# Performance work log

Hardware: AMD Instinct MI355X
Metric: run time of the kernel (lower is better)

Reference implementation:

```python
import jax, jax.numpy as jnp
import numpy as np

Nx, Nu, Ny, Np, H = 2, 1, 2, 8, 32
Nz = Np * (Nx + Nu)  # 24
B, T = 4096, 256
F, V, Delta = 0.1, 1.0, 1.0  # ps.squeeze(), volume, sample time
ymean = jnp.array([0.5, 0.5], jnp.float32)
ystd = jnp.array([0.3, 0.2], jnp.float32)
umean = jnp.array([1.0], jnp.float32)
ustd = jnp.array([0.5], jnp.float32)


def fnn(x, params):
    # dense layers: tanh hidden, linear output
    for W, b in params[:-1]:
        x = jnp.tanh(x @ W + b)
    W, b = params[-1]
    return x @ W + b


def fxzu(x, z, u, p1, p2, p3):
    # dCa/dt = F*(Caf-Ca)/V - r1 ; dCb/dt = -F*Cb/V + r1 - 3*r2 + r3
    Castd, Cbstd = ystd[0:1], ystd[1:2]
    r1 = fnn(x[:, 0:1], p1) * Castd
    r2 = fnn(x[:, 1:2], p2) * Cbstd
    r3 = fnn(z, p3) * Cbstd
    xs = x * ystd + ymean
    us = u * ustd + umean
    Ca, Cb, Caf = xs[:, 0:1], xs[:, 1:2], us[:, 0:1]
    dCa = F * (Caf - Ca) / V - r1
    dCb = -F * Cb / V + r1 - 3.0 * r2 + r3
    return jnp.concatenate([dCa, dCb], axis=-1) / ystd


def interp(yseq):
    # (B,(Np+1)*Nx) -> (B, Np*Nx): midpoints of consecutive Nx-blocks
    b = yseq.shape[0]
    y = yseq.reshape(b, Np + 1, Nx)
    return (0.5 * (y[:, :-1] + y[:, 1:])).reshape(b, Np * Nx)


def run(useq, xz0, p1, p2, p3):
    def step(xz, u):
        x, z = xz[:, :Nx], xz[:, Nx:]
        xpseq, upseq = z[:, :Np * Nx], z[:, Np * Nx:]
        k1 = fxzu(x, z, u, p1, p2, p3)
        z23 = jnp.concatenate([interp(jnp.concatenate([xpseq, x], -1)), upseq], -1)
        k2 = fxzu(x + Delta * k1 / 2, z23, u, p1, p2, p3)
        k3 = fxzu(x + Delta * k2 / 2, z23, u, p1, p2, p3)
        z4 = jnp.concatenate([xpseq[:, Nx:], x, upseq], -1)
        k4 = fxzu(x + Delta * k3, z4, u, p1, p2, p3)
        xplus = x + (Delta / 6.0) * (k1 + 2 * k2 + 2 * k3 + k4)
        zplus = jnp.concatenate([xpseq[:, Nx:], x, upseq[:, Nu:], u], -1)
        return jnp.concatenate([xplus, zplus], -1), x  # output is pre-update x
    _, ys = jax.lax.scan(step, xz0, jnp.swapaxes(useq, 0, 1))
    return jnp.swapaxes(ys, 0, 1)  # (B, T, Ny)


def setup_inputs() -> dict:
    key = jax.random.key(0)
    ks = jax.random.split(key, 12)
    inp = {
        'useq': jax.random.normal(ks[0], (B, T, Nu), jnp.float32),
        'xz0': jax.random.normal(ks[1], (B, Nx + Nz), jnp.float32),
    }
    dims = {'r1': [1, H, H, 1], 'r2': [1, H, H, 1], 'r3': [Nz, H, H, 1]}
    i = 2
    for name, ds in dims.items():
        for l, (din, dout) in enumerate(zip(ds[:-1], ds[1:])):
            inp[f'{name}W{l}'] = jax.random.normal(ks[i], (din, dout), jnp.float32) / np.sqrt(din).astype(np.float32)
            inp[f'{name}b{l}'] = jnp.zeros((dout,), jnp.float32)
            i += 1
    return inp


def reference(useq, xz0, r1W0, r1b0, r1W1, r1b1, r1W2, r1b2,
              r2W0, r2b0, r2W1, r2b1, r2W2, r2b2,
              r3W0, r3b0, r3W1, r3b1, r3W2, r3b2):
    p1 = [(r1W0, r1b0), (r1W1, r1b1), (r1W2, r1b2)]
    p2 = [(r2W0, r2b0), (r2W1, r2b1), (r2W2, r2b2)]
    p3 = [(r3W0, r3b0), (r3W1, r3b1), (r3W2, r3b2)]
    return run(useq, xz0, p1, p2, p3)
```

## Files before the change

### kernel.cpp

```cpp
#include <hip/hip_runtime.h>

#define DEVINL static __device__ __forceinline__
#define LDSBAR() asm volatile("s_waitcnt lgkmcnt(0)" ::: "memory")

typedef float v2f __attribute__((ext_vector_type(2)));

DEVINL v2f mk2(float a, float b) { v2f r; r.x = a; r.y = b; return r; }
DEVINL v2f pkfma(v2f a, v2f b, v2f c) { return __builtin_elementwise_fma(a, b, c); }

DEVINL float tanh_fast(float x) {
  float e = __expf(2.0f * x);
  return 1.0f - 2.0f * __builtin_amdgcn_rcpf(e + 1.0f);
}

template <int CTRL>
DEVINL float dpp_add(float v) {
  int t = __builtin_amdgcn_update_dpp(0, __float_as_int(v), CTRL, 0xF, 0xF, true);
  return v + __int_as_float(t);
}
DEVINL float rsum32(float v) {
  v = dpp_add<0xB1>(v);
  v = dpp_add<0x4E>(v);
  v = dpp_add<0x141>(v);
  v = dpp_add<0x140>(v);
  v += __int_as_float(__builtin_amdgcn_ds_swizzle(__float_as_int(v), 0x401F));
  return v;
}

DEVINL float dot32(const float* hrow, const v2f* W, float bias) {
  const float4* hp = (const float4*)hrow;
  v2f a0 = mk2(bias, 0.f), a1 = mk2(0.f, 0.f);
  v2f a2 = mk2(0.f, 0.f), a3 = mk2(0.f, 0.f);
#pragma unroll
  for (int q = 0; q < 8; q += 2) {
    float4 x = hp[q], y = hp[q + 1];
    a0 = pkfma(mk2(x.x, x.y), W[2 * q + 0], a0);
    a1 = pkfma(mk2(x.z, x.w), W[2 * q + 1], a1);
    a2 = pkfma(mk2(y.x, y.y), W[2 * q + 2], a2);
    a3 = pkfma(mk2(y.z, y.w), W[2 * q + 3], a3);
  }
  v2f s = (a0 + a1) + (a2 + a3);
  return s.x + s.y;
}
DEVINL float pdot16(const float* hrow, const v2f* W) {
  const float4* hp = (const float4*)hrow;
  v2f a0 = mk2(0.f, 0.f), a1 = mk2(0.f, 0.f);
  float4 x = hp[0], y = hp[1];
  a0 = pkfma(mk2(x.x, x.y), W[0], a0);
  a1 = pkfma(mk2(x.z, x.w), W[1], a1);
  a0 = pkfma(mk2(y.x, y.y), W[2], a0);
  a1 = pkfma(mk2(y.z, y.w), W[3], a1);
  x = hp[2]; y = hp[3];
  a0 = pkfma(mk2(x.x, x.y), W[4], a0);
  a1 = pkfma(mk2(x.z, x.w), W[5], a1);
  a0 = pkfma(mk2(y.x, y.y), W[6], a0);
  a1 = pkfma(mk2(y.z, y.w), W[7], a1);
  v2f s = a0 + a1;
  return s.x + s.y;
}

constexpr int TSTEPS = 256;

__global__ __launch_bounds__(64, 4) void reac_kernel(
    const float* __restrict__ useq,
    const float* __restrict__ xz0,
    const float* __restrict__ r1W0, const float* __restrict__ r1b0,
    const float* __restrict__ r1W1, const float* __restrict__ r1b1,
    const float* __restrict__ r1W2, const float* __restrict__ r1b2,
    const float* __restrict__ r2W0, const float* __restrict__ r2b0,
    const float* __restrict__ r2W1, const float* __restrict__ r2b1,
    const float* __restrict__ r2W2, const float* __restrict__ r2b2,
    const float* __restrict__ r3W0, const float* __restrict__ r3b0,
    const float* __restrict__ r3W1, const float* __restrict__ r3b1,
    const float* __restrict__ r3W2, const float* __restrict__ r3b2,
    float2* __restrict__ out)
{
  const int lane = threadIdx.x;
  const int j = lane & 31;
  const bool hi = lane >= 32;
  const int b = blockIdx.x;

  const float* W0p = hi ? r2W0 : r1W0;
  const float* B0p = hi ? r2b0 : r1b0;
  const float* W1p = hi ? r2W1 : r1W1;
  const float* B1p = hi ? r2b1 : r1b1;
  const float* W2p = hi ? r2W2 : r1W2;
  const float* B2p = hi ? r2b2 : r1b2;
  float w0 = W0p[j], b0 = B0p[j], b1 = B1p[j], w2 = W2p[j], b2 = B2p[0];
  float sc = hi ? 0.2f : 0.3f;

  v2f W1v[16];
#pragma unroll
  for (int k = 0; k < 16; ++k)
    W1v[k] = mk2(W1p[(2 * k) * 32 + j], W1p[(2 * k + 1) * 32 + j]);

  v2f W0Cv[12];
#pragma unroll
  for (int m = 0; m < 12; ++m)
    W0Cv[m] = mk2(r3W0[(2 * m) * 32 + j], r3W0[(2 * m + 1) * 32 + j]);
  const int kbase = hi ? 16 : 0;
  v2f W1Cv[8];
#pragma unroll
  for (int k = 0; k < 8; ++k)
    W1Cv[k] = mk2(r3W1[(kbase + 2 * k) * 32 + j],
                  r3W1[(kbase + 2 * k + 1) * 32 + j]);
  float b0C = r3b0[j], b1C = r3b1[j], w2C = r3W2[j], b2C = r3b2[0];

  __shared__ __align__(16) float zs[24];
  __shared__ __align__(16) float zb[16];
  __shared__ __align__(16) float h12[2][32];
  __shared__ __align__(16) float hR3[3][32];

  float x0 = xz0[b * 26 + 0];
  float x1 = xz0[b * 26 + 1];
  if (!hi && j < 24) zs[j] = xz0[b * 26 + 2 + j];
  LDSBAR();

  auto stage = [&](float sxv, float syv, float rc, float Caf,
                   float& kx, float& ky) {
    float s = hi ? syv : sxv;
    float h = tanh_fast(fmaf(s, w0, b0));
    LDSBAR();
    h12[hi][j] = h;
    LDSBAR();
    float a = dot32(&h12[hi][0], W1v, b1);
    float r = (rsum32(tanh_fast(a) * w2) + b2) * sc;
    float rp = __shfl_xor(r, 32);
    float ra = hi ? rp : r;
    float rb = hi ? r : rp;
    float Ca = fmaf(sxv, 0.3f, 0.5f);
    float Cb = fmaf(syv, 0.2f, 0.5f);
    float dCa = 0.1f * (Caf - Ca) - ra;
    float dCb = fmaf(-0.1f, Cb, ra - 3.0f * rb + rc);
    kx = dCa * (1.0f / 0.3f);
    ky = dCb * (1.0f / 0.2f);
  };

  float u = useq[b * TSTEPS];

  for (int t = 0; t < TSTEPS; ++t) {
    int tn = (t < TSTEPS - 1) ? (t + 1) : t;
    float u_nxt = useq[b * TSTEPS + tn];
    float Caf = fmaf(u, 0.5f, 1.0f);

    if (lane == 0) out[b * TSTEPS + t] = make_float2(x0, x1);

    if (!hi && j < 16) {
      zb[j] = (j < 14) ? zs[j + 2] : ((j == 14) ? x0 : x1);
    }
    LDSBAR();

    const float4* zp = (const float4*)(hi ? &zb[0] : &zs[0]);
    float4 z0 = zp[0], z1 = zp[1], z2 = zp[2], z3 = zp[3];
    const float4* up = (const float4*)&zs[16];
    float4 u0 = up[0], u1 = up[1];
    v2f aa = mk2(b0C, 0.f), ab = mk2(0.f, 0.f);
    aa = pkfma(mk2(z0.x, z0.y), W0Cv[0], aa);
    ab = pkfma(mk2(z0.z, z0.w), W0Cv[1], ab);
    aa = pkfma(mk2(z1.x, z1.y), W0Cv[2], aa);
    ab = pkfma(mk2(z1.z, z1.w), W0Cv[3], ab);
    aa = pkfma(mk2(z2.x, z2.y), W0Cv[4], aa);
    ab = pkfma(mk2(z2.z, z2.w), W0Cv[5], ab);
    aa = pkfma(mk2(z3.x, z3.y), W0Cv[6], aa);
    ab = pkfma(mk2(z3.z, z3.w), W0Cv[7], ab);
    aa = pkfma(mk2(u0.x, u0.y), W0Cv[8], aa);
    ab = pkfma(mk2(u0.z, u0.w), W0Cv[9], ab);
    aa = pkfma(mk2(u1.x, u1.y), W0Cv[10], aa);
    ab = pkfma(mk2(u1.z, u1.w), W0Cv[11], ab);
    v2f as = aa + ab;
    float A = as.x + as.y;
    float Ap = __shfl_xor(A, 32);
    float tA = tanh_fast(A);
    if (!hi) {
      hR3[0][j] = tA;
      hR3[1][j] = tanh_fast(0.5f * (A + Ap));
    } else {
      hR3[2][j] = tA;
    }
    LDSBAR();
    float p0 = pdot16(&hR3[0][kbase], W1Cv);
    float p1 = pdot16(&hR3[1][kbase], W1Cv);
    float p2 = pdot16(&hR3[2][kbase], W1Cv);
    float o0 = p0 + __shfl_xor(p0, 32) + b1C;
    float o1 = p1 + __shfl_xor(p1, 32) + b1C;
    float o2 = p2 + __shfl_xor(p2, 32) + b1C;
    float rc1  = (rsum32(tanh_fast(o0) * w2C) + b2C) * 0.2f;
    float rc23 = (rsum32(tanh_fast(o1) * w2C) + b2C) * 0.2f;
    float rc4  = (rsum32(tanh_fast(o2) * w2C) + b2C) * 0.2f;

    float kx1, ky1, kx2, ky2, kx3, ky3, kx4, ky4;
    stage(x0, x1, rc1, Caf, kx1, ky1);
    stage(fmaf(kx1, 0.5f, x0), fmaf(ky1, 0.5f, x1), rc23, Caf, kx2, ky2);
    stage(fmaf(kx2, 0.5f, x0), fmaf(ky2, 0.5f, x1), rc23, Caf, kx3, ky3);
    stage(x0 + kx3, x1 + ky3, rc4, Caf, kx4, ky4);

    float znew = 0.0f;
    bool updz = (!hi) && (j < 24);
    if (updz) znew = (j < 16) ? zb[j] : ((j < 23) ? zs[j + 1] : u);
    LDSBAR();
    if (updz) zs[j] = znew;
    x0 += (kx1 + 2.0f * (kx2 + kx3) + kx4) * (1.0f / 6.0f);
    x1 += (ky1 + 2.0f * (ky2 + ky3) + ky4) * (1.0f / 6.0f);
    u = u_nxt;
    LDSBAR();
  }
}

extern "C" void kernel_launch(void* const* d_in, const int* in_sizes, int n_in,
                              void* d_out, int out_size, void* d_ws, size_t ws_size,
                              hipStream_t stream) {
  const float* p[20];
  for (int i = 0; i < 20; ++i) p[i] = (const float*)d_in[i];
  reac_kernel<<<dim3(4096), dim3(64), 0, stream>>>(
      p[0], p[1], p[2], p[3], p[4], p[5], p[6], p[7], p[8], p[9], p[10],
      p[11], p[12], p[13], p[14], p[15], p[16], p[17], p[18], p[19],
      (float2*)d_out);
}
```

Measured before the change: 946.6 us.

## Fold tanh exp scaling into weights and drop explicit LDS waitcnt barriers

Pre-multiplies the layer weights and biases by 2*log2(e) so each tanh can call a raw exp2 builtin with no extra multiply. The output scales and affine constants are folded into w2/b2 and the Caf/Ca/Cb terms. The explicit s_waitcnt lgkmcnt(0) fences become compiler-only memory fences, so the compiler places its own waits, and shfl_xor is replaced by a direct ds_bpermute. It also switches to explicit waves_per_eu attributes; the risks are correctness of the intra-wave LDS ordering without explicit waits and small floating-point differences from the refactored arithmetic.

Result: faster. 871.6 us (-7.9%).

```diff
diff --git a/kernel.cpp b/kernel.cpp
--- a/kernel.cpp
+++ b/kernel.cpp
@@ -1,15 +1,23 @@
 #include <hip/hip_runtime.h>
 
 #define DEVINL static __device__ __forceinline__
-#define LDSBAR() asm volatile("s_waitcnt lgkmcnt(0)" ::: "memory")
+#define CFENCE() asm volatile("" ::: "memory")
 
 typedef float v2f __attribute__((ext_vector_type(2)));
 
 DEVINL v2f mk2(float a, float b) { v2f r; r.x = a; r.y = b; return r; }
 DEVINL v2f pkfma(v2f a, v2f b, v2f c) { return __builtin_elementwise_fma(a, b, c); }
 
-DEVINL float tanh_fast(float x) {
-  float e = __expf(2.0f * x);
+constexpr float KE = 2.885390081777927f;
+
+#if __has_builtin(__builtin_amdgcn_exp2f)
+DEVINL float exp2_fast(float x) { return __builtin_amdgcn_exp2f(x); }
+#else
+DEVINL float exp2_fast(float x) { return __expf(x * 0.6931471805599453f); }
+#endif
+
+DEVINL float tanh_pre(float t) {
+  float e = exp2_fast(t);
   return 1.0f - 2.0f * __builtin_amdgcn_rcpf(e + 1.0f);
 }
 
@@ -61,7 +69,8 @@
 
 constexpr int TSTEPS = 256;
 
-__global__ __launch_bounds__(64, 4) void reac_kernel(
+__global__ __attribute__((amdgpu_flat_work_group_size(64, 64)))
+__attribute__((amdgpu_waves_per_eu(4, 4))) void reac_kernel(
     const float* __restrict__ useq,
     const float* __restrict__ xz0,
     const float* __restrict__ r1W0, const float* __restrict__ r1b0,
@@ -79,6 +88,11 @@
   const int j = lane & 31;
   const bool hi = lane >= 32;
   const int b = blockIdx.x;
+  const int xaddr = ((lane ^ 32) << 2);
+
+  auto xchg = [&](float v) -> float {
+    return __int_as_float(__builtin_amdgcn_ds_bpermute(xaddr, __float_as_int(v)));
+  };
 
   const float* W0p = hi ? r2W0 : r1W0;
   const float* B0p = hi ? r2b0 : r1b0;
@@ -86,25 +100,29 @@
   const float* B1p = hi ? r2b1 : r1b1;
   const float* W2p = hi ? r2W2 : r1W2;
   const float* B2p = hi ? r2b2 : r1b2;
-  float w0 = W0p[j], b0 = B0p[j], b1 = B1p[j], w2 = W2p[j], b2 = B2p[0];
-  float sc = hi ? 0.2f : 0.3f;
+  const float sc = hi ? 0.2f : 0.3f;
+  float w0K = W0p[j] * KE, b0K = B0p[j] * KE;
+  float b1K = B1p[j] * KE;
+  float w2sc = W2p[j] * sc, b2sc = B2p[0] * sc;
 
   v2f W1v[16];
 #pragma unroll
   for (int k = 0; k < 16; ++k)
-    W1v[k] = mk2(W1p[(2 * k) * 32 + j], W1p[(2 * k + 1) * 32 + j]);
+    W1v[k] = mk2(W1p[(2 * k) * 32 + j] * KE, W1p[(2 * k + 1) * 32 + j] * KE);
 
   v2f W0Cv[12];
 #pragma unroll
   for (int m = 0; m < 12; ++m)
-    W0Cv[m] = mk2(r3W0[(2 * m) * 32 + j], r3W0[(2 * m + 1) * 32 + j]);
+    W0Cv[m] = mk2(r3W0[(2 * m) * 32 + j] * KE, r3W0[(2 * m + 1) * 32 + j] * KE);
   const int kbase = hi ? 16 : 0;
   v2f W1Cv[8];
 #pragma unroll
   for (int k = 0; k < 8; ++k)
-    W1Cv[k] = mk2(r3W1[(kbase + 2 * k) * 32 + j],
-                  r3W1[(kbase + 2 * k + 1) * 32 + j]);
-  float b0C = r3b0[j], b1C = r3b1[j], w2C = r3W2[j], b2C = r3b2[0];
+    W1Cv[k] = mk2(r3W1[(kbase + 2 * k) * 32 + j] * KE,
+                  r3W1[(kbase + 2 * k + 1) * 32 + j] * KE);
+  float b0CK = r3b0[j] * KE, b1CK = r3b1[j] * KE;
+  float w2C02 = r3W2[j] * 0.2f;
+  float b2Cs = r3b2[0] * 0.2f - 0.05f;
 
   __shared__ __align__(16) float zs[24];
   __shared__ __align__(16) float zb[16];
@@ -114,24 +132,22 @@
   float x0 = xz0[b * 26 + 0];
   float x1 = xz0[b * 26 + 1];
   if (!hi && j < 24) zs[j] = xz0[b * 26 + 2 + j];
-  LDSBAR();
-
-  auto stage = [&](float sxv, float syv, float rc, float Caf,
+  CFENCE();
+
+  auto stage = [&](float sxv, float syv, float rcp_, float CafF,
                    float& kx, float& ky) {
     float s = hi ? syv : sxv;
-    float h = tanh_fast(fmaf(s, w0, b0));
-    LDSBAR();
+    float h = tanh_pre(fmaf(s, w0K, b0K));
+    CFENCE();
     h12[hi][j] = h;
-    LDSBAR();
-    float a = dot32(&h12[hi][0], W1v, b1);
-    float r = (rsum32(tanh_fast(a) * w2) + b2) * sc;
-    float rp = __shfl_xor(r, 32);
+    CFENCE();
+    float a = dot32(&h12[hi][0], W1v, b1K);
+    float r = rsum32(tanh_pre(a) * w2sc) + b2sc;
+    float rp = xchg(r);
     float ra = hi ? rp : r;
     float rb = hi ? r : rp;
-    float Ca = fmaf(sxv, 0.3f, 0.5f);
-    float Cb = fmaf(syv, 0.2f, 0.5f);
-    float dCa = 0.1f * (Caf - Ca) - ra;
-    float dCb = fmaf(-0.1f, Cb, ra - 3.0f * rb + rc);
+    float dCa = fmaf(-0.03f, sxv, CafF) - ra;
+    float dCb = fmaf(-0.02f, syv, fmaf(-3.0f, rb, ra) + rcp_);
     kx = dCa * (1.0f / 0.3f);
     ky = dCb * (1.0f / 0.2f);
   };
@@ -141,20 +157,21 @@
   for (int t = 0; t < TSTEPS; ++t) {
     int tn = (t < TSTEPS - 1) ? (t + 1) : t;
     float u_nxt = useq[b * TSTEPS + tn];
-    float Caf = fmaf(u, 0.5f, 1.0f);
+    float CafF = fmaf(u, 0.05f, 0.05f);
 
     if (lane == 0) out[b * TSTEPS + t] = make_float2(x0, x1);
 
+    CFENCE();
     if (!hi && j < 16) {
       zb[j] = (j < 14) ? zs[j + 2] : ((j == 14) ? x0 : x1);
     }
-    LDSBAR();
+    CFENCE();
 
     const float4* zp = (const float4*)(hi ? &zb[0] : &zs[0]);
     float4 z0 = zp[0], z1 = zp[1], z2 = zp[2], z3 = zp[3];
     const float4* up = (const float4*)&zs[16];
     float4 u0 = up[0], u1 = up[1];
-    v2f aa = mk2(b0C, 0.f), ab = mk2(0.f, 0.f);
+    v2f aa = mk2(b0CK, 0.f), ab = mk2(0.f, 0.f);
     aa = pkfma(mk2(z0.x, z0.y), W0Cv[0], aa);
     ab = pkfma(mk2(z0.z, z0.w), W0Cv[1], ab);
     aa = pkfma(mk2(z1.x, z1.y), W0Cv[2], aa);
@@ -169,40 +186,40 @@
     ab = pkfma(mk2(u1.z, u1.w), W0Cv[11], ab);
     v2f as = aa + ab;
     float A = as.x + as.y;
-    float Ap = __shfl_xor(A, 32);
-    float tA = tanh_fast(A);
+    float Ap = xchg(A);
+    float tA = tanh_pre(A);
     if (!hi) {
       hR3[0][j] = tA;
-      hR3[1][j] = tanh_fast(0.5f * (A + Ap));
+      hR3[1][j] = tanh_pre(0.5f * (A + Ap));
     } else {
       hR3[2][j] = tA;
     }
-    LDSBAR();
+    CFENCE();
     float p0 = pdot16(&hR3[0][kbase], W1Cv);
     float p1 = pdot16(&hR3[1][kbase], W1Cv);
     float p2 = pdot16(&hR3[2][kbase], W1Cv);
-    float o0 = p0 + __shfl_xor(p0, 32) + b1C;
-    float o1 = p1 + __shfl_xor(p1, 32) + b1C;
-    float o2 = p2 + __shfl_xor(p2, 32) + b1C;
-    float rc1  = (rsum32(tanh_fast(o0) * w2C) + b2C) * 0.2f;
-    float rc23 = (rsum32(tanh_fast(o1) * w2C) + b2C) * 0.2f;
-    float rc4  = (rsum32(tanh_fast(o2) * w2C) + b2C) * 0.2f;
+    float o0 = p0 + xchg(p0) + b1CK;
+    float o1 = p1 + xchg(p1) + b1CK;
+    float o2 = p2 + xchg(p2) + b1CK;
+    float rc1  = rsum32(tanh_pre(o0) * w2C02) + b2Cs;
+    float rc23 = rsum32(tanh_pre(o1) * w2C02) + b2Cs;
+    float rc4  = rsum32(tanh_pre(o2) * w2C02) + b2Cs;
 
     float kx1, ky1, kx2, ky2, kx3, ky3, kx4, ky4;
-    stage(x0, x1, rc1, Caf, kx1, ky1);
-    stage(fmaf(kx1, 0.5f, x0), fmaf(ky1, 0.5f, x1), rc23, Caf, kx2, ky2);
-    stage(fmaf(kx2, 0.5f, x0), fmaf(ky2, 0.5f, x1), rc23, Caf, kx3, ky3);
-    stage(x0 + kx3, x1 + ky3, rc4, Caf, kx4, ky4);
+    stage(x0, x1, rc1, CafF, kx1, ky1);
+    stage(fmaf(kx1, 0.5f, x0), fmaf(ky1, 0.5f, x1), rc23, CafF, kx2, ky2);
+    stage(fmaf(kx2, 0.5f, x0), fmaf(ky2, 0.5f, x1), rc23, CafF, kx3, ky3);
+    stage(x0 + kx3, x1 + ky3, rc4, CafF, kx4, ky4);
 
     float znew = 0.0f;
     bool updz = (!hi) && (j < 24);
     if (updz) znew = (j < 16) ? zb[j] : ((j < 23) ? zs[j + 1] : u);
-    LDSBAR();
+    CFENCE();
     if (updz) zs[j] = znew;
     x0 += (kx1 + 2.0f * (kx2 + kx3) + kx4) * (1.0f / 6.0f);
     x1 += (ky1 + 2.0f * (ky2 + ky3) + ky4) * (1.0f / 6.0f);
     u = u_nxt;
-    LDSBAR();
+    CFENCE();
   }
 }
 
```
